# Kernel tuning notes

Measured on AMD Instinct MI355X. Metric: run time of the kernel, lower is better.

## Reference

```python
import jax, jax.numpy as jnp
import numpy as np

B, T, D = 8, 2048, 1024
H, N = 8, 32  # n_heads, n_state


def _xavier(key, shape, fan_in, fan_out):
    lim = float(np.sqrt(6.0 / (fan_in + fan_out)))
    return jax.random.uniform(key, shape, jnp.float32, -lim, lim)


def setup_inputs() -> dict:
    key = jax.random.key(0)
    ks = jax.random.split(key, 8)
    x = jax.random.normal(ks[0], (B, T, D), jnp.float32)
    W_in = _xavier(ks[1], (D, D), D, D)                    # in_proj.weight [d_inner, dim]
    # per-head xavier on [n_state, d_inner] slices -> limit sqrt(6/(N+D))
    W_k = _xavier(ks[2], (H * N, D), N, D)
    W_v = _xavier(ks[3], (H * N, D), N, D)
    W_q = _xavier(ks[4], (H * N, D), N, D)
    W_beta = _xavier(ks[5], (H * N, D), N, D)
    b_beta = jnp.full((H, N), 2.0, jnp.float32)            # init_beta_bias
    W_out = _xavier(ks[6], (D, H * N), H * N, D)           # out_proj.weight [dim, H*n]
    return {"x": x, "W_in": W_in, "W_k": W_k, "W_v": W_v, "W_q": W_q,
            "W_beta": W_beta, "b_beta": b_beta, "W_out": W_out}


def reference(x, W_in, W_k, W_v, W_q, W_beta, b_beta, W_out):
    b, t, d = x.shape
    h, n = b_beta.shape
    # in_proj + SiLU (use_conv=False)
    xp = jax.nn.silu(jnp.einsum('btd,ed->bte', x, W_in))   # [B,T,D_inner]
    def proj(W):  # -> [T,B,H,N]
        return jnp.einsum('btd,md->btm', xp, W).reshape(b, t, h, n).transpose(1, 0, 2, 3)
    k_all = proj(W_k)
    v_all = proj(W_v)
    q_all = proj(W_q)
    beta_all = jax.nn.sigmoid(proj(W_beta) + b_beta)       # [T,B,H,N]

    S0 = jnp.zeros((b, h, n, n), x.dtype)

    def step(S, inp):
        k, v, q, beta = inp                                 # each [B,H,N]
        kn = k / (jnp.linalg.norm(k, axis=-1, keepdims=True) + 1e-6)
        retrieved = jnp.einsum('bhij,bhj->bhi', S, kn)
        delta = v - retrieved
        S = jnp.tanh(beta[..., None] * S + delta[..., None] * kn[..., None, :])
        Sq = jnp.einsum('bhij,bhj->bhi', S, q)
        out = Sq * jax.nn.silu(Sq)                          # [B,H,N]
        return S, out

    S_final, outs = jax.lax.scan(step, S0, (k_all, v_all, q_all, beta_all))
    cell_out = outs.transpose(1, 0, 2, 3).reshape(b, t, h * n)  # [B,T,H*N]
    y = jnp.einsum('btm,dm->btd', cell_out, W_out)          # out_proj, no bias
    return y, S_final
```

## Files before the change

kernel.cpp:

```cpp
#include <hip/hip_runtime.h>
#include <hip/hip_bf16.h>

#define TT 2048
#define BB 8
#define HH 8
#define NNS 32
#define MM (BB * TT)
#define CH 16

typedef __attribute__((ext_vector_type(8))) short short8;
typedef __attribute__((ext_vector_type(4))) float f32x4;

__device__ __forceinline__ float bf2f(ushort u) {
    return __uint_as_float(((unsigned)u) << 16);
}
__device__ __forceinline__ ushort f2bf(float f) {
    unsigned x = __float_as_uint(f);
    unsigned r = (x + 0x7fffu + ((x >> 16) & 1u)) >> 16;
    return (ushort)r;
}
__device__ __forceinline__ float sigmoidf_fast(float x) {
    float e = __builtin_amdgcn_exp2f(x * -1.4426950408889634f);
    return __builtin_amdgcn_rcpf(1.0f + e);
}
__device__ __forceinline__ float tanhf_fast(float x) {
    float e = __builtin_amdgcn_exp2f(x * 2.8853900817779268f);
    return fmaf(-2.0f, __builtin_amdgcn_rcpf(e + 1.0f), 1.0f);
}

template<int CTRL>
__device__ __forceinline__ float dpp_add(float x) {
    int y = __builtin_amdgcn_update_dpp(0, __float_as_int(x), CTRL, 0xF, 0xF, true);
    return x + __int_as_float(y);
}
__device__ __forceinline__ float red16(float x) {
    x = dpp_add<0xB1>(x);
    x = dpp_add<0x4E>(x);
    x = dpp_add<0x124>(x);
    x = dpp_add<0x128>(x);
    return x;
}

__device__ __forceinline__ void stage8_split(const float* __restrict__ src,
                                             ushort* __restrict__ hi,
                                             ushort* __restrict__ lo) {
    float4 x0 = *reinterpret_cast<const float4*>(src);
    float4 x1 = *reinterpret_cast<const float4*>(src + 4);
    float xs[8] = {x0.x, x0.y, x0.z, x0.w, x1.x, x1.y, x1.z, x1.w};
    ushort h[8], l[8];
#pragma unroll
    for (int i = 0; i < 8; ++i) {
        ushort hh = f2bf(xs[i]);
        h[i] = hh;
        l[i] = f2bf(xs[i] - bf2f(hh));
    }
    *reinterpret_cast<uint4*>(hi) = *reinterpret_cast<const uint4*>(h);
    *reinterpret_cast<uint4*>(lo) = *reinterpret_cast<const uint4*>(l);
}
__device__ __forceinline__ void stage8_hi(const float* __restrict__ src,
                                          ushort* __restrict__ hi) {
    float4 x0 = *reinterpret_cast<const float4*>(src);
    float4 x1 = *reinterpret_cast<const float4*>(src + 4);
    float xs[8] = {x0.x, x0.y, x0.z, x0.w, x1.x, x1.y, x1.z, x1.w};
    ushort h[8];
#pragma unroll
    for (int i = 0; i < 8; ++i) h[i] = f2bf(xs[i]);
    *reinterpret_cast<uint4*>(hi) = *reinterpret_cast<const uint4*>(h);
}

template<int ACT>
__global__ __launch_bounds__(256) void gemm_split(
    const float* __restrict__ A,
    const float* __restrict__ W0, const float* __restrict__ W1,
    const float* __restrict__ W2, const float* __restrict__ W3,
    const float* __restrict__ bbeta,
    float* __restrict__ C, int M, int N, int K)
{
    __shared__ __align__(16) ushort Ah[64][40], Al[64][40];
    __shared__ __align__(16) ushort Wh[64][40], Wl[64][40];
    const int n0 = blockIdx.x * 64;
    const int m0 = blockIdx.y * 64;
    const int t  = threadIdx.x;
    const int wave = t >> 6, lane = t & 63;
    const int lr = lane & 15, lq = lane >> 4;

    const float* Wsel;
    {
        int wi = n0 >> 8;
        Wsel = (wi == 0) ? W0 : (wi == 1) ? W1 : (wi == 2) ? W2 : W3;
    }
    const int wr0 = n0 & 255;
    const int ar = t >> 2;
    const int ak = (t & 3) * 8;

    f32x4 acc[4];
#pragma unroll
    for (int c = 0; c < 4; ++c) acc[c] = (f32x4){0.f, 0.f, 0.f, 0.f};

    for (int k0 = 0; k0 < K; k0 += 32) {
        __syncthreads();
        stage8_split(&A[(size_t)(m0 + ar) * K + k0 + ak], &Ah[ar][ak], &Al[ar][ak]);
        stage8_split(&Wsel[(size_t)(wr0 + ar) * K + k0 + ak], &Wh[ar][ak], &Wl[ar][ak]);
        __syncthreads();
        short8 ah = *reinterpret_cast<const short8*>(&Ah[wave * 16 + lr][lq * 8]);
        short8 al = *reinterpret_cast<const short8*>(&Al[wave * 16 + lr][lq * 8]);
#pragma unroll
        for (int c = 0; c < 4; ++c) {
            short8 bh = *reinterpret_cast<const short8*>(&Wh[c * 16 + lr][lq * 8]);
            short8 bl = *reinterpret_cast<const short8*>(&Wl[c * 16 + lr][lq * 8]);
            acc[c] = __builtin_amdgcn_mfma_f32_16x16x32_bf16(ah, bh, acc[c], 0, 0, 0);
            acc[c] = __builtin_amdgcn_mfma_f32_16x16x32_bf16(ah, bl, acc[c], 0, 0, 0);
            acc[c] = __builtin_amdgcn_mfma_f32_16x16x32_bf16(al, bh, acc[c], 0, 0, 0);
        }
    }

#pragma unroll
    for (int c = 0; c < 4; ++c) {
#pragma unroll
        for (int r2 = 0; r2 < 4; ++r2) {
            int mg = m0 + wave * 16 + lq * 4 + r2;
            int ng = n0 + c * 16 + lr;
            float v = acc[c][r2];
            if (ACT == 1) v = v * sigmoidf_fast(v);
            if (ACT == 2 && ng >= 768) v = sigmoidf_fast(v + bbeta[ng - 768]);
            C[(size_t)mg * N + ng] = v;
        }
    }
}

__global__ __launch_bounds__(256) void gemm_bf_a(
    const ushort* __restrict__ A,
    const float* __restrict__ W0, const float* __restrict__ W1,
    const float* __restrict__ W2, const float* __restrict__ W3,
    float* __restrict__ C, int M, int N, int K)
{
    __shared__ __align__(16) ushort As[64][40];
    __shared__ __align__(16) ushort Ws[64][40];
    const int n0 = blockIdx.x * 64;
    const int m0 = blockIdx.y * 64;
    const int t  = threadIdx.x;
    const int wave = t >> 6, lane = t & 63;
    const int lr = lane & 15, lq = lane >> 4;

    const float* Wsel;
    {
        int wi = n0 >> 8;
        Wsel = (wi == 0) ? W0 : (wi == 1) ? W1 : (wi == 2) ? W2 : W3;
    }
    const int wr0 = n0 & 255;
    const int ar = t >> 2;
    const int ak = (t & 3) * 8;

    f32x4 acc[4];
#pragma unroll
    for (int c = 0; c < 4; ++c) acc[c] = (f32x4){0.f, 0.f, 0.f, 0.f};

    for (int k0 = 0; k0 < K; k0 += 32) {
        __syncthreads();
        *reinterpret_cast<uint4*>(&As[ar][ak]) =
            *reinterpret_cast<const uint4*>(&A[(size_t)(m0 + ar) * K + k0 + ak]);
        stage8_hi(&Wsel[(size_t)(wr0 + ar) * K + k0 + ak], &Ws[ar][ak]);
        __syncthreads();
        short8 af = *reinterpret_cast<const short8*>(&As[wave * 16 + lr][lq * 8]);
#pragma unroll
        for (int c = 0; c < 4; ++c) {
            short8 bfv = *reinterpret_cast<const short8*>(&Ws[c * 16 + lr][lq * 8]);
            acc[c] = __builtin_amdgcn_mfma_f32_16x16x32_bf16(af, bfv, acc[c], 0, 0, 0);
        }
    }

#pragma unroll
    for (int c = 0; c < 4; ++c) {
#pragma unroll
        for (int r2 = 0; r2 < 4; ++r2) {
            int mg = m0 + wave * 16 + lq * 4 + r2;
            int ng = n0 + c * 16 + lr;
            C[(size_t)mg * N + ng] = acc[c][r2];
        }
    }
}

__global__ __launch_bounds__(256) void kn_kernel(
    const float* __restrict__ P, float* __restrict__ KN)
{
    int idx = blockIdx.x * 256 + threadIdx.x;
    int col = idx & 255;
    int bt  = idx >> 8;
    float k = P[(size_t)bt * 1024 + col];
    float ks = k * k;
    ks += __shfl_xor(ks, 1, 32);  ks += __shfl_xor(ks, 2, 32);
    ks += __shfl_xor(ks, 4, 32);  ks += __shfl_xor(ks, 8, 32);
    ks += __shfl_xor(ks, 16, 32);
    KN[idx] = k * __builtin_amdgcn_rcpf(sqrtf(ks) + 1e-6f);
}

template<int DO_STAGE>
__device__ __forceinline__ void scan_chunk(
    float (&K_)[CH][32], float (&Q_)[CH][32], float (&V_)[CH][4], float (&B_)[CH][4],
    float (&NK)[CH][32], float (&NQ)[CH][32], float (&NV)[CH][4], float (&NB)[CH][4],
    const float*& gkn, const float*& gq, const float*& gv, const float*& gb,
    float (&rk0)[4], float (&rk1)[4], float (&rq0)[4], float (&rq1)[4],
    float (&rv)[4], float (&rb)[4],
    float& S0, float& S1, float& osv,
    ushort* __restrict__ cell, size_t crow,
    int l, int iw, int j)
{
    float4 Lk0, Lk1, Lq0, Lq1;
    float Lv = 0.f, Lb = 0.f;
    if (DO_STAGE) {
        Lk0 = *reinterpret_cast<const float4*>(gkn);
        Lk1 = *reinterpret_cast<const float4*>(gkn + 8 * 256);
        Lq0 = *reinterpret_cast<const float4*>(gq);
        Lq1 = *reinterpret_cast<const float4*>(gq + 8 * 1024);
        Lv  = *gv;
        Lb  = *gb;
        gkn += CH * 256; gq += CH * 1024; gv += CH * 1024; gb += CH * 1024;
    }
#pragma unroll
    for (int tl = 0; tl < CH; ++tl) {
        if (tl < CH - 2) {
            const int dn = (tl + 2) & 3;
            rk0[dn] = K_[tl + 2][l];   rk1[dn] = K_[tl + 2][l + 16];
            rq0[dn] = Q_[tl + 2][l];   rq1[dn] = Q_[tl + 2][l + 16];
            rv[dn]  = V_[tl + 2][iw];  rb[dn]  = B_[tl + 2][iw];
        }
        const int sl = tl & 3;
        float p = red16(fmaf(S0, rk0[sl], S1 * rk1[sl]));
        float delta = rv[sl] - p;
        S0 = tanhf_fast(fmaf(rb[sl], S0, delta * rk0[sl]));
        S1 = tanhf_fast(fmaf(rb[sl], S1, delta * rk1[sl]));
        float sq = red16(fmaf(S0, rq0[sl], S1 * rq1[sl]));
        osv = (l == (tl & 7)) ? sq : osv;
        if ((tl & 7) == 7 && l < 8) {
            float o = osv * osv * sigmoidf_fast(osv);
            cell[crow + (size_t)(tl - 7 + l) * 256] = f2bf(o);
        }
    }
    if (DO_STAGE) {
        *reinterpret_cast<float4*>(&NK[j >> 3][(j & 7) * 4]) = Lk0;
        *reinterpret_cast<float4*>(&NK[8 + (j >> 3)][(j & 7) * 4]) = Lk1;
        *reinterpret_cast<float4*>(&NQ[j >> 3][(j & 7) * 4]) = Lq0;
        *reinterpret_cast<float4*>(&NQ[8 + (j >> 3)][(j & 7) * 4]) = Lq1;
        NV[j >> 2][j & 3] = Lv;
        NB[j >> 2][j & 3] = Lb;
#pragma unroll
        for (int d = 0; d < 2; ++d) {
            rk0[d] = NK[d][l];  rk1[d] = NK[d][l + 16];
            rq0[d] = NQ[d][l];  rq1[d] = NQ[d][l + 16];
            rv[d]  = NV[d][iw]; rb[d]  = NB[d][iw];
        }
    }
}

__global__ __launch_bounds__(64, 1) void scan_kernel(
    const float* __restrict__ P,
    const float* __restrict__ KN,
    ushort* __restrict__ cell,
    float* __restrict__ Sout)
{
    const int b    = blockIdx.x & 7;
    const int r    = blockIdx.x >> 3;
    const int h    = r & 7;
    const int quad = r >> 3;
    const int j    = threadIdx.x;
    const int l    = j & 15;
    const int iw   = j >> 4;
    const int i    = quad * 4 + iw;

    __shared__ __align__(16) float sKN0[CH][32], sKN1[CH][32];
    __shared__ __align__(16) float sQ0[CH][32],  sQ1[CH][32];
    __shared__ __align__(16) float sV0[CH][4],   sV1[CH][4];
    __shared__ __align__(16) float sB0[CH][4],   sB1[CH][4];

    const size_t bt0 = (size_t)b * TT;
    const float* gkn = KN + (bt0 + (j >> 3)) * 256 + h * 32 + (j & 7) * 4;
    const float* gq  = P  + (bt0 + (j >> 3)) * 1024 + 512 + h * 32 + (j & 7) * 4;
    const float* gv  = P  + (bt0 + (j >> 2)) * 1024 + 256 + h * 32 + quad * 4 + (j & 3);
    const float* gb  = P  + (bt0 + (j >> 2)) * 1024 + 768 + h * 32 + quad * 4 + (j & 3);

    float rk0[4], rk1[4], rq0[4], rq1[4], rv[4], rb[4];
    float S0 = 0.f, S1 = 0.f, osv = 0.f;
    const size_t cb = (size_t)b * TT * 256 + h * 32 + i;

    {
        float4 k0 = *reinterpret_cast<const float4*>(gkn);
        float4 k1 = *reinterpret_cast<const float4*>(gkn + 8 * 256);
        float4 q0 = *reinterpret_cast<const float4*>(gq);
        float4 q1 = *reinterpret_cast<const float4*>(gq + 8 * 1024);
        float v0 = *gv, b0 = *gb;
        gkn += CH * 256; gq += CH * 1024; gv += CH * 1024; gb += CH * 1024;
        *reinterpret_cast<float4*>(&sKN0[j >> 3][(j & 7) * 4]) = k0;
        *reinterpret_cast<float4*>(&sKN0[8 + (j >> 3)][(j & 7) * 4]) = k1;
        *reinterpret_cast<float4*>(&sQ0[j >> 3][(j & 7) * 4]) = q0;
        *reinterpret_cast<float4*>(&sQ0[8 + (j >> 3)][(j & 7) * 4]) = q1;
        sV0[j >> 2][j & 3] = v0;
        sB0[j >> 2][j & 3] = b0;
#pragma unroll
        for (int d = 0; d < 2; ++d) {
            rk0[d] = sKN0[d][l];  rk1[d] = sKN0[d][l + 16];
            rq0[d] = sQ0[d][l];   rq1[d] = sQ0[d][l + 16];
            rv[d]  = sV0[d][iw];  rb[d]  = sB0[d][iw];
        }
    }

    size_t crow = cb;
    for (int c = 0; c < 126; c += 2) {
        scan_chunk<1>(sKN0, sQ0, sV0, sB0, sKN1, sQ1, sV1, sB1,
                      gkn, gq, gv, gb, rk0, rk1, rq0, rq1, rv, rb,
                      S0, S1, osv, cell, crow, l, iw, j);
        crow += (size_t)CH * 256;
        scan_chunk<1>(sKN1, sQ1, sV1, sB1, sKN0, sQ0, sV0, sB0,
                      gkn, gq, gv, gb, rk0, rk1, rq0, rq1, rv, rb,
                      S0, S1, osv, cell, crow, l, iw, j);
        crow += (size_t)CH * 256;
    }
    scan_chunk<1>(sKN0, sQ0, sV0, sB0, sKN1, sQ1, sV1, sB1,
                  gkn, gq, gv, gb, rk0, rk1, rq0, rq1, rv, rb,
                  S0, S1, osv, cell, crow, l, iw, j);
    crow += (size_t)CH * 256;
    scan_chunk<0>(sKN1, sQ1, sV1, sB1, sKN0, sQ0, sV0, sB0,
                  gkn, gq, gv, gb, rk0, rk1, rq0, rq1, rv, rb,
                  S0, S1, osv, cell, crow, l, iw, j);

    float* so = Sout + (((size_t)(b * HH + h)) * NNS + i) * NNS;
    so[l] = S0;
    so[l + 16] = S1;
}

extern "C" void kernel_launch(void* const* d_in, const int* in_sizes, int n_in,
                              void* d_out, int out_size, void* d_ws, size_t ws_size,
                              hipStream_t stream) {
    const float* x     = (const float*)d_in[0];
    const float* W_in  = (const float*)d_in[1];
    const float* W_k   = (const float*)d_in[2];
    const float* W_v   = (const float*)d_in[3];
    const float* W_q   = (const float*)d_in[4];
    const float* W_b   = (const float*)d_in[5];
    const float* b_b   = (const float*)d_in[6];
    const float* W_out = (const float*)d_in[7];
    float* out = (float*)d_out;

    const int M = MM;
    float*  xp   = (float*)d_ws;
    float*  P    = xp + (size_t)M * 1024;
    float*  KN   = P  + (size_t)M * 1024;
    ushort* cell = (ushort*)(KN + (size_t)M * 256);

    dim3 blk(256);
    dim3 g1(1024 / 64, M / 64);

    gemm_split<1><<<g1, blk, 0, stream>>>(x, W_in, W_in + 256 * 1024,
                                          W_in + 512 * 1024, W_in + 768 * 1024,
                                          b_b, xp, M, 1024, 1024);
    gemm_split<2><<<g1, blk, 0, stream>>>(xp, W_k, W_v, W_q, W_b,
                                          b_b, P, M, 1024, 1024);
    kn_kernel<<<dim3((M * 256) / 256), blk, 0, stream>>>(P, KN);
    scan_kernel<<<dim3(512), dim3(64), 0, stream>>>(P, KN, cell, out + (size_t)M * 1024);
    gemm_bf_a<<<g1, blk, 0, stream>>>(cell, W_out, W_out + 256 * 256,
                                      W_out + 512 * 256, W_out + 768 * 256,
                                      out, M, 1024, 256);
}
```

Before: 684.7 us.

## Batch scan steps in groups of eight, deferring Sq reductions off the critical path

Restructures the serial scan so each 16-step chunk runs as two groups of eight steps. Operands for a group are loaded from LDS in bulk, one group ahead. The per-step Sq reduction, which does not feed the recurrence, is now deferred and done for all eight steps together after the group, taking cross-lane shuffles off the dependent chain. V and beta are packed into one shared array. The cost is many more live registers, which may spill or hurt scheduling.

Result: no change. 677.9 us (-1.0%).

```diff
diff --git a/kernel.cpp b/kernel.cpp
--- a/kernel.cpp
+++ b/kernel.cpp
@@ -194,16 +194,66 @@
     KN[idx] = k * __builtin_amdgcn_rcpf(sqrtf(ks) + 1e-6f);
 }
 
+__device__ __forceinline__ void lds_load8(
+    float (&K_)[CH][32], float (&Q_)[CH][32], float (&VB)[CH][8],
+    int base, int l, int iw,
+    float (&k0)[8], float (&k1)[8], float (&q0)[8], float (&q1)[8],
+    float (&vv)[8], float (&bb)[8])
+{
+#pragma unroll
+    for (int u = 0; u < 8; ++u) {
+        k0[u] = K_[base + u][l];  k1[u] = K_[base + u][l + 16];
+        q0[u] = Q_[base + u][l];  q1[u] = Q_[base + u][l + 16];
+        vv[u] = VB[base + u][iw]; bb[u] = VB[base + u][iw + 4];
+    }
+}
+
+__device__ __forceinline__ void steps8(
+    float (&k0)[8], float (&k1)[8], float (&q0)[8], float (&q1)[8],
+    float (&vv)[8], float (&bb)[8],
+    float& S0, float& S1, float (&sqp)[8])
+{
+#pragma unroll
+    for (int u = 0; u < 8; ++u) {
+        float p = red16(fmaf(S0, k0[u], S1 * k1[u]));
+        float delta = vv[u] - p;
+        S0 = tanhf_fast(fmaf(bb[u], S0, delta * k0[u]));
+        S1 = tanhf_fast(fmaf(bb[u], S1, delta * k1[u]));
+        sqp[u] = fmaf(S0, q0[u], S1 * q1[u]);
+    }
+}
+
+__device__ __forceinline__ void flush8(
+    float (&sqp)[8], ushort* __restrict__ cell, size_t crow, int l)
+{
+    float r0 = red16(sqp[0]), r1 = red16(sqp[1]);
+    float r2 = red16(sqp[2]), r3 = red16(sqp[3]);
+    float r4 = red16(sqp[4]), r5 = red16(sqp[5]);
+    float r6 = red16(sqp[6]), r7 = red16(sqp[7]);
+    if (l < 8) {
+        float s01 = (l & 1) ? r1 : r0;
+        float s23 = (l & 1) ? r3 : r2;
+        float s45 = (l & 1) ? r5 : r4;
+        float s67 = (l & 1) ? r7 : r6;
+        float a03 = (l & 2) ? s23 : s01;
+        float a47 = (l & 2) ? s67 : s45;
+        float sel = (l & 4) ? a47 : a03;
+        float o = sel * sel * sigmoidf_fast(sel);
+        cell[crow + (size_t)l * 256] = f2bf(o);
+    }
+}
+
 template<int DO_STAGE>
-__device__ __forceinline__ void scan_chunk(
-    float (&K_)[CH][32], float (&Q_)[CH][32], float (&V_)[CH][4], float (&B_)[CH][4],
-    float (&NK)[CH][32], float (&NQ)[CH][32], float (&NV)[CH][4], float (&NB)[CH][4],
+__device__ __forceinline__ void scan_chunk16(
+    float (&K_)[CH][32], float (&Q_)[CH][32], float (&VB)[CH][8],
+    float (&NK)[CH][32], float (&NQ)[CH][32], float (&NVB)[CH][8],
     const float*& gkn, const float*& gq, const float*& gv, const float*& gb,
-    float (&rk0)[4], float (&rk1)[4], float (&rq0)[4], float (&rq1)[4],
-    float (&rv)[4], float (&rb)[4],
-    float& S0, float& S1, float& osv,
-    ushort* __restrict__ cell, size_t crow,
-    int l, int iw, int j)
+    float (&k0A)[8], float (&k1A)[8], float (&q0A)[8], float (&q1A)[8],
+    float (&vvA)[8], float (&bbA)[8],
+    float (&k0B)[8], float (&k1B)[8], float (&q0B)[8], float (&q1B)[8],
+    float (&vvB)[8], float (&bbB)[8],
+    float& S0, float& S1, float (&sqp)[8],
+    ushort* __restrict__ cell, size_t crow, int l, int iw, int j)
 {
     float4 Lk0, Lk1, Lq0, Lq1;
     float Lv = 0.f, Lb = 0.f;
@@ -216,40 +266,20 @@
         Lb  = *gb;
         gkn += CH * 256; gq += CH * 1024; gv += CH * 1024; gb += CH * 1024;
     }
-#pragma unroll
-    for (int tl = 0; tl < CH; ++tl) {
-        if (tl < CH - 2) {
-            const int dn = (tl + 2) & 3;
-            rk0[dn] = K_[tl + 2][l];   rk1[dn] = K_[tl + 2][l + 16];
-            rq0[dn] = Q_[tl + 2][l];   rq1[dn] = Q_[tl + 2][l + 16];
-            rv[dn]  = V_[tl + 2][iw];  rb[dn]  = B_[tl + 2][iw];
-        }
-        const int sl = tl & 3;
-        float p = red16(fmaf(S0, rk0[sl], S1 * rk1[sl]));
-        float delta = rv[sl] - p;
-        S0 = tanhf_fast(fmaf(rb[sl], S0, delta * rk0[sl]));
-        S1 = tanhf_fast(fmaf(rb[sl], S1, delta * rk1[sl]));
-        float sq = red16(fmaf(S0, rq0[sl], S1 * rq1[sl]));
-        osv = (l == (tl & 7)) ? sq : osv;
-        if ((tl & 7) == 7 && l < 8) {
-            float o = osv * osv * sigmoidf_fast(osv);
-            cell[crow + (size_t)(tl - 7 + l) * 256] = f2bf(o);
-        }
-    }
+    lds_load8(K_, Q_, VB, 8, l, iw, k0B, k1B, q0B, q1B, vvB, bbB);
+    steps8(k0A, k1A, q0A, q1A, vvA, bbA, S0, S1, sqp);
+    flush8(sqp, cell, crow, l);
     if (DO_STAGE) {
         *reinterpret_cast<float4*>(&NK[j >> 3][(j & 7) * 4]) = Lk0;
         *reinterpret_cast<float4*>(&NK[8 + (j >> 3)][(j & 7) * 4]) = Lk1;
         *reinterpret_cast<float4*>(&NQ[j >> 3][(j & 7) * 4]) = Lq0;
         *reinterpret_cast<float4*>(&NQ[8 + (j >> 3)][(j & 7) * 4]) = Lq1;
-        NV[j >> 2][j & 3] = Lv;
-        NB[j >> 2][j & 3] = Lb;
-#pragma unroll
-        for (int d = 0; d < 2; ++d) {
-            rk0[d] = NK[d][l];  rk1[d] = NK[d][l + 16];
-            rq0[d] = NQ[d][l];  rq1[d] = NQ[d][l + 16];
-            rv[d]  = NV[d][iw]; rb[d]  = NB[d][iw];
-        }
-    }
+        NVB[j >> 2][j & 3] = Lv;
+        NVB[j >> 2][4 + (j & 3)] = Lb;
+        lds_load8(NK, NQ, NVB, 0, l, iw, k0A, k1A, q0A, q1A, vvA, bbA);
+    }
+    steps8(k0B, k1B, q0B, q1B, vvB, bbB, S0, S1, sqp);
+    flush8(sqp, cell, crow + (size_t)8 * 256, l);
 }
 
 __global__ __launch_bounds__(64, 1) void scan_kernel(
@@ -267,10 +297,9 @@
     const int iw   = j >> 4;
     const int i    = quad * 4 + iw;
 
-    __shared__ __align__(16) float sKN0[CH][32], sKN1[CH][32];
-    __shared__ __align__(16) float sQ0[CH][32],  sQ1[CH][32];
-    __shared__ __align__(16) float sV0[CH][4],   sV1[CH][4];
-    __shared__ __align__(16) float sB0[CH][4],   sB1[CH][4];
+    __shared__ __align__(16) float sK0[CH][32], sK1[CH][32];
+    __shared__ __align__(16) float sQ0[CH][32], sQ1[CH][32];
+    __shared__ __align__(16) float sVB0[CH][8], sVB1[CH][8];
 
     const size_t bt0 = (size_t)b * TT;
     const float* gkn = KN + (bt0 + (j >> 3)) * 256 + h * 32 + (j & 7) * 4;
@@ -278,49 +307,54 @@
     const float* gv  = P  + (bt0 + (j >> 2)) * 1024 + 256 + h * 32 + quad * 4 + (j & 3);
     const float* gb  = P  + (bt0 + (j >> 2)) * 1024 + 768 + h * 32 + quad * 4 + (j & 3);
 
-    float rk0[4], rk1[4], rq0[4], rq1[4], rv[4], rb[4];
-    float S0 = 0.f, S1 = 0.f, osv = 0.f;
+    float k0A[8], k1A[8], q0A[8], q1A[8], vvA[8], bbA[8];
+    float k0B[8], k1B[8], q0B[8], q1B[8], vvB[8], bbB[8];
+    float sqp[8];
+    float S0 = 0.f, S1 = 0.f;
     const size_t cb = (size_t)b * TT * 256 + h * 32 + i;
 
     {
-        float4 k0 = *reinterpret_cast<const float4*>(gkn);
-        float4 k1 = *reinterpret_cast<const float4*>(gkn + 8 * 256);
-        float4 q0 = *reinterpret_cast<const float4*>(gq);
-        float4 q1 = *reinterpret_cast<const float4*>(gq + 8 * 1024);
+        float4 K0v = *reinterpret_cast<const float4*>(gkn);
+        float4 K1v = *reinterpret_cast<const float4*>(gkn + 8 * 256);
+        float4 Q0v = *reinterpret_cast<const float4*>(gq);
+        float4 Q1v = *reinterpret_cast<const float4*>(gq + 8 * 1024);
         float v0 = *gv, b0 = *gb;
         gkn += CH * 256; gq += CH * 1024; gv += CH * 1024; gb += CH * 1024;
-        *reinterpret_cast<float4*>(&sKN0[j >> 3][(j & 7) * 4]) = k0;
-        *reinterpret_cast<float4*>(&sKN0[8 + (j >> 3)][(j & 7) * 4]) = k1;
-        *reinterpret_cast<float4*>(&sQ0[j >> 3][(j & 7) * 4]) = q0;
-        *reinterpret_cast<float4*>(&sQ0[8 + (j >> 3)][(j & 7) * 4]) = q1;
-        sV0[j >> 2][j & 3] = v0;
-        sB0[j >> 2][j & 3] = b0;
-#pragma unroll
-        for (int d = 0; d < 2; ++d) {
-            rk0[d] = sKN0[d][l];  rk1[d] = sKN0[d][l + 16];
-            rq0[d] = sQ0[d][l];   rq1[d] = sQ0[d][l + 16];
-            rv[d]  = sV0[d][iw];  rb[d]  = sB0[d][iw];
-        }
-    }
+        *reinterpret_cast<float4*>(&sK0[j >> 3][(j & 7) * 4]) = K0v;
+        *reinterpret_cast<float4*>(&sK0[8 + (j >> 3)][(j & 7) * 4]) = K1v;
+        *reinterpret_cast<float4*>(&sQ0[j >> 3][(j & 7) * 4]) = Q0v;
+        *reinterpret_cast<float4*>(&sQ0[8 + (j >> 3)][(j & 7) * 4]) = Q1v;
+        sVB0[j >> 2][j & 3] = v0;
+        sVB0[j >> 2][4 + (j & 3)] = b0;
+    }
+    lds_load8(sK0, sQ0, sVB0, 0, l, iw, k0A, k1A, q0A, q1A, vvA, bbA);
 
     size_t crow = cb;
-    for (int c = 0; c < 126; c += 2) {
-        scan_chunk<1>(sKN0, sQ0, sV0, sB0, sKN1, sQ1, sV1, sB1,
-                      gkn, gq, gv, gb, rk0, rk1, rq0, rq1, rv, rb,
-                      S0, S1, osv, cell, crow, l, iw, j);
+    for (int c = 0; c < 63; ++c) {
+        scan_chunk16<1>(sK0, sQ0, sVB0, sK1, sQ1, sVB1,
+                        gkn, gq, gv, gb,
+                        k0A, k1A, q0A, q1A, vvA, bbA,
+                        k0B, k1B, q0B, q1B, vvB, bbB,
+                        S0, S1, sqp, cell, crow, l, iw, j);
         crow += (size_t)CH * 256;
-        scan_chunk<1>(sKN1, sQ1, sV1, sB1, sKN0, sQ0, sV0, sB0,
-                      gkn, gq, gv, gb, rk0, rk1, rq0, rq1, rv, rb,
-                      S0, S1, osv, cell, crow, l, iw, j);
+        scan_chunk16<1>(sK1, sQ1, sVB1, sK0, sQ0, sVB0,
+                        gkn, gq, gv, gb,
+                        k0A, k1A, q0A, q1A, vvA, bbA,
+                        k0B, k1B, q0B, q1B, vvB, bbB,
+                        S0, S1, sqp, cell, crow, l, iw, j);
         crow += (size_t)CH * 256;
     }
-    scan_chunk<1>(sKN0, sQ0, sV0, sB0, sKN1, sQ1, sV1, sB1,
-                  gkn, gq, gv, gb, rk0, rk1, rq0, rq1, rv, rb,
-                  S0, S1, osv, cell, crow, l, iw, j);
+    scan_chunk16<1>(sK0, sQ0, sVB0, sK1, sQ1, sVB1,
+                    gkn, gq, gv, gb,
+                    k0A, k1A, q0A, q1A, vvA, bbA,
+                    k0B, k1B, q0B, q1B, vvB, bbB,
+                    S0, S1, sqp, cell, crow, l, iw, j);
     crow += (size_t)CH * 256;
-    scan_chunk<0>(sKN1, sQ1, sV1, sB1, sKN0, sQ0, sV0, sB0,
-                  gkn, gq, gv, gb, rk0, rk1, rq0, rq1, rv, rb,
-                  S0, S1, osv, cell, crow, l, iw, j);
+    scan_chunk16<0>(sK1, sQ1, sVB1, sK0, sQ0, sVB0,
+                    gkn, gq, gv, gb,
+                    k0A, k1A, q0A, q1A, vvA, bbA,
+                    k0B, k1B, q0B, q1B, vvB, bbB,
+                    S0, S1, sqp, cell, crow, l, iw, j);
 
     float* so = Sout + (((size_t)(b * HH + h)) * NNS + i) * NNS;
     so[l] = S0;
```
